# Optimization experiments

Measured on AMD Instinct MI355X. Metric: run time of the kernel, lower is better.

Reference implementation:

```python
import jax, jax.numpy as jnp
import numpy as np

NUM_HEADS = 16


def setup_inputs() -> dict:
    key = jax.random.key(0)
    ks = jax.random.split(key, 4)
    B, C, T, D = 1, 1, 3072, 1024
    s = 1.0 / np.sqrt(D)
    return {
        "x": jax.random.normal(ks[0], (B, C, T, D), dtype=jnp.float32),
        "Wq": jax.random.normal(ks[1], (D, D), dtype=jnp.float32) * s,
        "bq": jnp.zeros((D,), dtype=jnp.float32),
        "Wk": jax.random.normal(ks[2], (D, D), dtype=jnp.float32) * s,
        "bk": jnp.zeros((D,), dtype=jnp.float32),
        "Wv": jax.random.normal(ks[3], (D, D), dtype=jnp.float32) * s,
        "bv": jnp.zeros((D,), dtype=jnp.float32),
        "gamma": jnp.float32(0.5),  # learned scalar; 0.0 at torch init, nonzero here for a meaningful signal
    }


def reference(x, Wq, bq, Wk, bk, Wv, bv, gamma):
    # x: (B, C, T, D); Linear acts on last dim (torch: y = x @ W.T + b)
    B, C, T, D = x.shape
    H = NUM_HEADS
    q = (jnp.einsum("bctd,ed->bcte", x, Wq) + bq).reshape(B, -1, T, H)  # (B, X, T, H), X = C*D/H
    k = (jnp.einsum("bctd,ed->bcte", x, Wk) + bk).reshape(B, -1, T, H)
    v = (jnp.einsum("bctd,ed->bcte", x, Wv) + bv).reshape(B, -1, T, H)
    q = q.transpose(0, 3, 2, 1)  # (B, H, T, X)
    k = k.transpose(0, 3, 1, 2)  # (B, H, X, T)
    energy = q @ k               # (B, H, T, T)  -- note: NO 1/sqrt(d) scaling, as in source
    attn = jax.nn.softmax(energy, axis=-1)
    v = v.transpose(0, 3, 2, 1)  # (B, H, T, X)
    out = attn @ v               # (B, H, T, X)
    out = out.transpose(0, 2, 3, 1).reshape(B, T, -1)  # (B, T, X*H) = (B, T, C*D)
    # residual broadcast: (B, T, C*D) + (B, C, T, D); valid since B == C == 1
    return gamma * out + x
```

## Files before the change

### kernel.cpp

```cpp
#include <hip/hip_runtime.h>


typedef _Float16 v8h __attribute__((ext_vector_type(8)));
typedef _Float16 v4h __attribute__((ext_vector_type(4)));
typedef __fp16   v2pk __attribute__((ext_vector_type(2)));
typedef __fp16   v4pk __attribute__((ext_vector_type(4)));
typedef float    v4f __attribute__((ext_vector_type(4)));

#define TSEQ 3072
#define DM   1024
#define NH   16
#define XD   64
#define LOG2E 1.44269504f

__device__ __forceinline__ void async_load16(const void* g, void* l) {
  __builtin_amdgcn_global_load_lds(
      (const __attribute__((address_space(1))) unsigned int*)g,
      (__attribute__((address_space(3))) unsigned int*)l,
      16, 0, 0);
}

__device__ __forceinline__ float fexp2(float x) {
  float r; asm("v_exp_f32 %0, %1" : "=v"(r) : "v"(x)); return r;
}
__device__ __forceinline__ float flog2(float x) {
  float r; asm("v_log_f32 %0, %1" : "=v"(r) : "v"(x)); return r;
}

extern "C" __global__ __launch_bounds__(256) void cvt_kernel(
    const float* __restrict__ x, const float* __restrict__ wq,
    const float* __restrict__ wk, const float* __restrict__ wv,
    _Float16* __restrict__ xb, _Float16* __restrict__ wb)
{
  const int NX4 = (TSEQ * DM) / 4;
  const int NT  = NX4 * 2;
  for (int i = blockIdx.x * blockDim.x + threadIdx.x; i < NT;
       i += gridDim.x * blockDim.x) {
    float4 v;
    _Float16* dst;
    if (i < NX4) {
      v = ((const float4*)x)[i];
      dst = xb + (size_t)i * 4;
    } else {
      const int j = i - NX4;
      const int n = j >> 8;
      if (n < 1024)      v = ((const float4*)wq)[j];
      else if (n < 2048) v = ((const float4*)wk)[j - 262144];
      else               v = ((const float4*)wv)[j - 524288];
      dst = wb + (size_t)j * 4;
    }
    v4h h;
    h[0] = (_Float16)v.x; h[1] = (_Float16)v.y;
    h[2] = (_Float16)v.z; h[3] = (_Float16)v.w;
    *(v4h*)dst = h;
  }
}

extern "C" __global__ __launch_bounds__(256) void qkv_gemm_kernel(
    const _Float16* __restrict__ xb, const _Float16* __restrict__ wb,
    const float* __restrict__ bq, const float* __restrict__ bk,
    const float* __restrict__ bv,
    _Float16* __restrict__ qlin, _Float16* __restrict__ klin,
    _Float16* __restrict__ vlin)
{
  __shared__ _Float16 As[128 * 32];
  __shared__ _Float16 Bs[128 * 32];
  const int tid = threadIdx.x;
  const int w = tid >> 6, l = tid & 63;
  const int li = l & 15, lg = l >> 4;
  const int wm = w >> 1, wn = w & 1;
  const int bid = blockIdx.x;
  const int swz = (bid & 7) * 72 + (bid >> 3);
  const int m0 = (swz / 24) * 128, n0 = (swz % 24) * 128;
  v4f acc[4][4] = {};
  const int srow = l >> 2;
  const int scol = (l & 3) * 8;
  for (int k0 = 0; k0 < DM; k0 += 32) {
#pragma unroll
    for (int c = 0; c < 2; ++c) {
      const int rbase = c * 64 + w * 16;
      async_load16(xb + (size_t)(m0 + rbase + srow) * DM + k0 + scol, &As[rbase * 32]);
      async_load16(wb + (size_t)(n0 + rbase + srow) * DM + k0 + scol, &Bs[rbase * 32]);
    }
    __syncthreads();
    v8h af[4], bf[4];
#pragma unroll
    for (int mi = 0; mi < 4; ++mi)
      af[mi] = *(const v8h*)&As[(wm * 64 + mi * 16 + li) * 32 + lg * 8];
#pragma unroll
    for (int ni = 0; ni < 4; ++ni)
      bf[ni] = *(const v8h*)&Bs[(wn * 64 + ni * 16 + li) * 32 + lg * 8];
#pragma unroll
    for (int mi = 0; mi < 4; ++mi)
#pragma unroll
      for (int ni = 0; ni < 4; ++ni)
        acc[mi][ni] = __builtin_amdgcn_mfma_f32_16x16x32_f16(
            af[mi], bf[ni], acc[mi][ni], 0, 0, 0);
    __syncthreads();
  }
  const int which = n0 >> 10;
  const int ebase = n0 & 1023;
  const float* bias = which == 0 ? bq : (which == 1 ? bk : bv);
  _Float16* outp = which == 0 ? qlin : (which == 1 ? klin : vlin);
#pragma unroll
  for (int mi = 0; mi < 4; ++mi)
#pragma unroll
    for (int r = 0; r < 4; ++r) {
      const int t = m0 + wm * 64 + mi * 16 + lg * 4 + r;
#pragma unroll
      for (int ni = 0; ni < 4; ++ni) {
        const int e = ebase + wn * 64 + ni * 16 + li;
        outp[(size_t)t * DM + e] = (_Float16)(acc[mi][ni][r] + bias[e]);
      }
    }
}

extern "C" __global__ __launch_bounds__(256) void repack_kernel(
    const _Float16* __restrict__ qlin, const _Float16* __restrict__ klin,
    const _Float16* __restrict__ vlin,
    _Float16* __restrict__ qh, _Float16* __restrict__ kh,
    _Float16* __restrict__ vt)
{
  const int NE = NH * TSEQ * XD;
  for (int g = blockIdx.x * blockDim.x + threadIdx.x; g < 3 * NE;
       g += gridDim.x * blockDim.x) {
    if (g < 2 * NE) {
      const int gg = (g < NE) ? g : g - NE;
      const int xx = gg & 63;
      const int rest = gg >> 6;
      const int h = rest / TSEQ;
      const int i = rest - h * TSEQ;
      const int t = xx * 48 + (i >> 6);
      const int e = ((i & 63) << 4) + h;
      if (g < NE) qh[gg] = qlin[t * DM + e];
      else        kh[gg] = (_Float16)((float)klin[t * DM + e] * LOG2E);
    } else {
      const int o = g - 2 * NE;
      const int j = o % TSEQ;
      const int rest = o / TSEQ;
      const int xx = rest & 63;
      const int h = rest >> 6;
      const int t = xx * 48 + (j >> 6);
      const int e = ((j & 63) << 4) + h;
      vt[o] = vlin[t * DM + e];
    }
  }
}

extern "C" __global__ __launch_bounds__(512, 2) void attn_kernel(
    const _Float16* __restrict__ qh, const _Float16* __restrict__ kh,
    const _Float16* __restrict__ vt,
    _Float16* __restrict__ oP0, _Float16* __restrict__ oP1,
    float* __restrict__ sml0, float* __restrict__ sml1)
{
  __shared__ _Float16 SH[8192];
  const int tid = threadIdx.x;
  const int w = tid >> 6, l = tid & 63;
  const int li = l & 15, lg = l >> 4;
  const int b = blockIdx.x;
  const int r = b >> 3;
  const int head = (b & 7) + 8 * (r & 1);
  const int qt = (r >> 1) & 7;
  const int jh = r >> 4;
  const int i0 = qt * 384;
  const size_t hb = (size_t)head * TSEQ * XD;
  _Float16* oPart = jh ? oP1 : oP0;
  float* smlp = jh ? sml1 : sml0;

  v8h qf[3][2];
#pragma unroll
  for (int ct = 0; ct < 3; ++ct) {
    const _Float16* qrow = qh + hb + (size_t)(i0 + w * 48 + ct * 16 + li) * XD;
    qf[ct][0] = *(const v8h*)(qrow + lg * 8);
    qf[ct][1] = *(const v8h*)(qrow + 32 + lg * 8);
  }
  float m2[3] = {24.0f * LOG2E, 24.0f * LOG2E, 24.0f * LOG2E};
  float l4[3] = {0.0f, 0.0f, 0.0f};
  v4f oacc[4][3] = {};
  const int r8 = l >> 3, c8 = l & 7;
  const int jbase = jh * 1536;

  for (int j0 = jbase; j0 < jbase + 1536; j0 += 64) {
    {
      const int row = w * 8 + r8;
      async_load16(kh + hb + (size_t)(j0 + row) * XD + ((c8 ^ (row & 7)) * 8),
                   &SH[w * 512]);
      async_load16(vt + hb + (size_t)row * TSEQ + j0 + ((c8 ^ (row & 7)) * 8),
                   &SH[4096 + w * 512]);
    }
    __syncthreads();
    const _Float16* Kc = &SH[0];
    const _Float16* Vc = &SH[4096];

    v4f e4[3][4];
#pragma unroll
    for (int kt = 0; kt < 4; ++kt) {
      const int krow = kt * 16 + li;
      const v8h kf0 = *(const v8h*)&Kc[krow * 64 + ((lg ^ (li & 7)) * 8)];
      const v8h kf1 = *(const v8h*)&Kc[krow * 64 + (((4 + lg) ^ (li & 7)) * 8)];
#pragma unroll
      for (int ct = 0; ct < 3; ++ct) {
        v4f a = {-m2[ct], -m2[ct], -m2[ct], -m2[ct]};
        a = __builtin_amdgcn_mfma_f32_16x16x32_f16(kf0, qf[ct][0], a, 0, 0, 0);
        a = __builtin_amdgcn_mfma_f32_16x16x32_f16(kf1, qf[ct][1], a, 0, 0, 0);
        e4[ct][kt] = a;
      }
    }

    float gm = -1.0e30f;
#pragma unroll
    for (int ct = 0; ct < 3; ++ct)
#pragma unroll
      for (int kt = 0; kt < 4; ++kt)
        gm = fmaxf(fmaxf(gm, fmaxf(e4[ct][kt][0], e4[ct][kt][1])),
                   fmaxf(e4[ct][kt][2], e4[ct][kt][3]));
    if (__any(gm > 11.5f)) {
#pragma unroll
      for (int ct = 0; ct < 3; ++ct) {
        float rm = -1.0e30f;
#pragma unroll
        for (int kt = 0; kt < 4; ++kt)
          rm = fmaxf(fmaxf(rm, fmaxf(e4[ct][kt][0], e4[ct][kt][1])),
                     fmaxf(e4[ct][kt][2], e4[ct][kt][3]));
        rm = fmaxf(rm, __shfl_xor(rm, 16, 64));
        rm = fmaxf(rm, __shfl_xor(rm, 32, 64));
        rm = fmaxf(rm, 0.0f);
        const float fs = fexp2(-rm);
#pragma unroll
        for (int kt = 0; kt < 4; ++kt)
#pragma unroll
          for (int rr = 0; rr < 4; ++rr) e4[ct][kt][rr] -= rm;
        l4[ct] *= fs;
#pragma unroll
        for (int mi = 0; mi < 4; ++mi) oacc[mi][ct] *= fs;
        m2[ct] += rm;
      }
    }

    v4h pv[3][4];
#pragma unroll
    for (int ct = 0; ct < 3; ++ct) {
#pragma unroll
      for (int kt = 0; kt < 4; ++kt) {
        const float p0 = fexp2(e4[ct][kt][0]);
        const float p1 = fexp2(e4[ct][kt][1]);
        const float p2 = fexp2(e4[ct][kt][2]);
        const float p3 = fexp2(e4[ct][kt][3]);
        const v2pk lo = __builtin_amdgcn_cvt_pkrtz(p0, p1);
        const v2pk hi = __builtin_amdgcn_cvt_pkrtz(p2, p3);
        const v4pk pk = __builtin_shufflevector(lo, hi, 0, 1, 2, 3);
        pv[ct][kt] = __builtin_bit_cast(v4h, pk);
        l4[ct] += (p0 + p1) + (p2 + p3);
      }
    }

#pragma unroll
    for (int mi = 0; mi < 4; ++mi) {
      const int vrow = mi * 16 + li;
      const int vb = vrow * 64 + (lg & 1) * 4;
#pragma unroll
      for (int kt = 0; kt < 4; ++kt) {
        const v4h vf = *(const v4h*)&Vc[vb + (((kt * 2 + (lg >> 1)) ^ (li & 7)) * 8)];
#pragma unroll
        for (int ct = 0; ct < 3; ++ct)
          oacc[mi][ct] = __builtin_amdgcn_mfma_f32_16x16x16f16(
              vf, pv[ct][kt], oacc[mi][ct], 0, 0, 0);
      }
    }
    __syncthreads();
  }

#pragma unroll
  for (int ct = 0; ct < 3; ++ct) {
    float ls = l4[ct];
    ls += __shfl_xor(ls, 16, 64);
    ls += __shfl_xor(ls, 32, 64);
    const float inv = 1.0f / ls;
    const int rl = w * 48 + ct * 16 + li;
    if (lg == 0) smlp[(size_t)(i0 + rl) * NH + head] = m2[ct] + flog2(ls);
#pragma unroll
    for (int mi = 0; mi < 4; ++mi) {
      v4h o4;
#pragma unroll
      for (int rr = 0; rr < 4; ++rr) o4[rr] = (_Float16)(oacc[mi][ct][rr] * inv);
      *(v4h*)&oPart[(size_t)(i0 + rl) * DM + head * 64 + mi * 16 + lg * 4] = o4;
    }
  }
}

extern "C" __global__ __launch_bounds__(256) void epilogue_kernel(
    const _Float16* __restrict__ oP0, const _Float16* __restrict__ oP1,
    const float* __restrict__ sml0, const float* __restrict__ sml1,
    const float* __restrict__ xin, const float* __restrict__ gscal,
    float* __restrict__ outp)
{
  __shared__ float po[8 * 1024];
  const int tid = threadIdx.x;
  const size_t t0 = (size_t)blockIdx.x * 8;
  {
    const int tr = tid >> 5;
    const int c0 = (tid & 31) * 32;
    const int h = c0 >> 6;
    const size_t t = t0 + tr;
    const float s0 = sml0[t * NH + h], s1 = sml1[t * NH + h];
    const float M = fmaxf(s0, s1);
    float u0 = fexp2(s0 - M), u1 = fexp2(s1 - M);
    const float dn = 1.0f / (u0 + u1);
    u0 *= dn; u1 *= dn;
    const _Float16* p0 = oP0 + t * DM + c0;
    const _Float16* p1 = oP1 + t * DM + c0;
#pragma unroll
    for (int c = 0; c < 4; ++c) {
      const v8h a = *(const v8h*)(p0 + c * 8);
      const v8h bb = *(const v8h*)(p1 + c * 8);
#pragma unroll
      for (int e = 0; e < 8; ++e)
        po[tr * 1024 + c0 + c * 8 + e] = u0 * (float)a[e] + u1 * (float)bb[e];
    }
  }
  __syncthreads();
  const float g = gscal[0];
  const int tr = tid >> 5;
  const int d0 = (tid & 31) * 32;
  const size_t rb = (t0 + tr) * DM + d0;
#pragma unroll
  for (int c4 = 0; c4 < 8; ++c4) {
    const float4 xi = *(const float4*)&xin[rb + c4 * 4];
    float4 rr;
    rr.x = g * po[tr * 1024 + ((c4 * 4 + 0) & 15) * 64 + ((d0 + c4 * 4 + 0) >> 4)] + xi.x;
    rr.y = g * po[tr * 1024 + ((c4 * 4 + 1) & 15) * 64 + ((d0 + c4 * 4 + 1) >> 4)] + xi.y;
    rr.z = g * po[tr * 1024 + ((c4 * 4 + 2) & 15) * 64 + ((d0 + c4 * 4 + 2) >> 4)] + xi.z;
    rr.w = g * po[tr * 1024 + ((c4 * 4 + 3) & 15) * 64 + ((d0 + c4 * 4 + 3) >> 4)] + xi.w;
    *(float4*)&outp[rb + c4 * 4] = rr;
  }
}

extern "C" void kernel_launch(void* const* d_in, const int* in_sizes, int n_in,
                              void* d_out, int out_size, void* d_ws, size_t ws_size,
                              hipStream_t stream)
{
  const float* x  = (const float*)d_in[0];
  const float* Wq = (const float*)d_in[1];
  const float* bq = (const float*)d_in[2];
  const float* Wk = (const float*)d_in[3];
  const float* bk = (const float*)d_in[4];
  const float* Wv = (const float*)d_in[5];
  const float* bv = (const float*)d_in[6];
  const float* gm = (const float*)d_in[7];
  float* outp = (float*)d_out;
  char* ws = (char*)d_ws;
  const size_t SZH = (size_t)TSEQ * DM * sizeof(_Float16);
  _Float16* xb   = (_Float16*)(ws);
  _Float16* wb   = (_Float16*)(ws + SZH);
  _Float16* qlin = (_Float16*)(ws + 2 * SZH);
  _Float16* klin = (_Float16*)(ws + 3 * SZH);
  _Float16* vlin = (_Float16*)(ws + 4 * SZH);
  _Float16* qhp  = (_Float16*)(ws + 5 * SZH);
  _Float16* khp  = (_Float16*)(ws + 6 * SZH);
  _Float16* vtp  = (_Float16*)(ws + 7 * SZH);
  _Float16* oP0  = (_Float16*)(ws);
  _Float16* oP1  = (_Float16*)(ws + SZH);
  float*    sml0 = (float*)(ws + 3 * SZH);
  float*    sml1 = sml0 + (size_t)TSEQ * NH;

  cvt_kernel<<<dim3(1024), dim3(256), 0, stream>>>(x, Wq, Wk, Wv, xb, wb);
  qkv_gemm_kernel<<<dim3(576), dim3(256), 0, stream>>>(xb, wb, bq, bk, bv,
                                                       qlin, klin, vlin);
  repack_kernel<<<dim3(4096), dim3(256), 0, stream>>>(qlin, klin, vlin,
                                                      qhp, khp, vtp);
  attn_kernel<<<dim3(256), dim3(512), 0, stream>>>(qhp, khp, vtp,
                                                   oP0, oP1, sml0, sml1);
  epilogue_kernel<<<dim3(384), dim3(256), 0, stream>>>(oP0, oP1, sml0, sml1,
                                                       x, gm, outp);
  (void)in_sizes; (void)n_in; (void)out_size; (void)ws_size;
}
```

Measured before the change: 137.7 us.

## Fuse head repack into QKV GEMM epilogue and halve attention block size

The QKV GEMM epilogue now writes Q, K (pre-scaled by log2e) and transposed V straight into the per-head attention layouts, so the separate repack kernel and its intermediate buffers are gone. This removes one launch and a full read-write pass over the Q/K/V tensors, at the cost of scattered, uncoalesced stores from the GEMM. The attention kernel also moves from 512-thread blocks over 384 query rows to 256-thread blocks over 192 rows, with twice as many blocks and each thread issuing two async K/V tile loads. The workspace layout is adjusted so the softmax statistics buffers reuse the freed space.

Result: slower. 180.9 us (+31.4%).

```diff
diff --git a/kernel.cpp b/kernel.cpp
--- a/kernel.cpp
+++ b/kernel.cpp
@@ -60,8 +60,8 @@
     const _Float16* __restrict__ xb, const _Float16* __restrict__ wb,
     const float* __restrict__ bq, const float* __restrict__ bk,
     const float* __restrict__ bv,
-    _Float16* __restrict__ qlin, _Float16* __restrict__ klin,
-    _Float16* __restrict__ vlin)
+    _Float16* __restrict__ qh, _Float16* __restrict__ kh,
+    _Float16* __restrict__ vt)
 {
   __shared__ _Float16 As[128 * 32];
   __shared__ _Float16 Bs[128 * 32];
@@ -101,53 +101,31 @@
   const int which = n0 >> 10;
   const int ebase = n0 & 1023;
   const float* bias = which == 0 ? bq : (which == 1 ? bk : bv);
-  _Float16* outp = which == 0 ? qlin : (which == 1 ? klin : vlin);
+  const float scale = (which == 1) ? LOG2E : 1.0f;
+  const int h = li;
 #pragma unroll
   for (int mi = 0; mi < 4; ++mi)
 #pragma unroll
     for (int r = 0; r < 4; ++r) {
       const int t = m0 + wm * 64 + mi * 16 + lg * 4 + r;
+      const int tq = t / 48;
+      const int ib = (t - tq * 48) * 64;
 #pragma unroll
       for (int ni = 0; ni < 4; ++ni) {
         const int e = ebase + wn * 64 + ni * 16 + li;
-        outp[(size_t)t * DM + e] = (_Float16)(acc[mi][ni][r] + bias[e]);
-      }
-    }
-}
-
-extern "C" __global__ __launch_bounds__(256) void repack_kernel(
-    const _Float16* __restrict__ qlin, const _Float16* __restrict__ klin,
-    const _Float16* __restrict__ vlin,
-    _Float16* __restrict__ qh, _Float16* __restrict__ kh,
-    _Float16* __restrict__ vt)
-{
-  const int NE = NH * TSEQ * XD;
-  for (int g = blockIdx.x * blockDim.x + threadIdx.x; g < 3 * NE;
-       g += gridDim.x * blockDim.x) {
-    if (g < 2 * NE) {
-      const int gg = (g < NE) ? g : g - NE;
-      const int xx = gg & 63;
-      const int rest = gg >> 6;
-      const int h = rest / TSEQ;
-      const int i = rest - h * TSEQ;
-      const int t = xx * 48 + (i >> 6);
-      const int e = ((i & 63) << 4) + h;
-      if (g < NE) qh[gg] = qlin[t * DM + e];
-      else        kh[gg] = (_Float16)((float)klin[t * DM + e] * LOG2E);
-    } else {
-      const int o = g - 2 * NE;
-      const int j = o % TSEQ;
-      const int rest = o / TSEQ;
-      const int xx = rest & 63;
-      const int h = rest >> 6;
-      const int t = xx * 48 + (j >> 6);
-      const int e = ((j & 63) << 4) + h;
-      vt[o] = vlin[t * DM + e];
-    }
-  }
-}
-
-extern "C" __global__ __launch_bounds__(512, 2) void attn_kernel(
+        const int colq = (ebase >> 4) + wn * 4 + ni;
+        const float v = (acc[mi][ni][r] + bias[e]) * scale;
+        if (which == 2)
+          vt[((size_t)h * XD + tq) * TSEQ + ib + colq] = (_Float16)v;
+        else if (which == 0)
+          qh[(size_t)h * TSEQ * XD + (size_t)(ib + colq) * XD + tq] = (_Float16)v;
+        else
+          kh[(size_t)h * TSEQ * XD + (size_t)(ib + colq) * XD + tq] = (_Float16)v;
+      }
+    }
+}
+
+extern "C" __global__ __launch_bounds__(256, 2) void attn_kernel(
     const _Float16* __restrict__ qh, const _Float16* __restrict__ kh,
     const _Float16* __restrict__ vt,
     _Float16* __restrict__ oP0, _Float16* __restrict__ oP1,
@@ -158,11 +136,11 @@
   const int w = tid >> 6, l = tid & 63;
   const int li = l & 15, lg = l >> 4;
   const int b = blockIdx.x;
-  const int r = b >> 3;
-  const int head = (b & 7) + 8 * (r & 1);
-  const int qt = (r >> 1) & 7;
-  const int jh = r >> 4;
-  const int i0 = qt * 384;
+  const int rest = b >> 3;
+  const int head = (b & 7) + 8 * (rest & 1);
+  const int qt = (rest >> 1) & 15;
+  const int jh = rest >> 5;
+  const int i0 = qt * 192;
   const size_t hb = (size_t)head * TSEQ * XD;
   _Float16* oPart = jh ? oP1 : oP0;
   float* smlp = jh ? sml1 : sml0;
@@ -181,12 +159,14 @@
   const int jbase = jh * 1536;
 
   for (int j0 = jbase; j0 < jbase + 1536; j0 += 64) {
-    {
-      const int row = w * 8 + r8;
+#pragma unroll
+    for (int s = 0; s < 2; ++s) {
+      const int n = w * 2 + s;
+      const int row = n * 8 + r8;
       async_load16(kh + hb + (size_t)(j0 + row) * XD + ((c8 ^ (row & 7)) * 8),
-                   &SH[w * 512]);
+                   &SH[n * 512]);
       async_load16(vt + hb + (size_t)row * TSEQ + j0 + ((c8 ^ (row & 7)) * 8),
-                   &SH[4096 + w * 512]);
+                   &SH[4096 + n * 512]);
     }
     __syncthreads();
     const _Float16* Kc = &SH[0];
@@ -352,23 +332,18 @@
   const size_t SZH = (size_t)TSEQ * DM * sizeof(_Float16);
   _Float16* xb   = (_Float16*)(ws);
   _Float16* wb   = (_Float16*)(ws + SZH);
-  _Float16* qlin = (_Float16*)(ws + 2 * SZH);
-  _Float16* klin = (_Float16*)(ws + 3 * SZH);
-  _Float16* vlin = (_Float16*)(ws + 4 * SZH);
+  float*    sml0 = (float*)(ws + 2 * SZH);
+  float*    sml1 = sml0 + (size_t)TSEQ * NH;
   _Float16* qhp  = (_Float16*)(ws + 5 * SZH);
   _Float16* khp  = (_Float16*)(ws + 6 * SZH);
   _Float16* vtp  = (_Float16*)(ws + 7 * SZH);
   _Float16* oP0  = (_Float16*)(ws);
   _Float16* oP1  = (_Float16*)(ws + SZH);
-  float*    sml0 = (float*)(ws + 3 * SZH);
-  float*    sml1 = sml0 + (size_t)TSEQ * NH;
 
   cvt_kernel<<<dim3(1024), dim3(256), 0, stream>>>(x, Wq, Wk, Wv, xb, wb);
   qkv_gemm_kernel<<<dim3(576), dim3(256), 0, stream>>>(xb, wb, bq, bk, bv,
-                                                       qlin, klin, vlin);
-  repack_kernel<<<dim3(4096), dim3(256), 0, stream>>>(qlin, klin, vlin,
-                                                      qhp, khp, vtp);
-  attn_kernel<<<dim3(256), dim3(512), 0, stream>>>(qhp, khp, vtp,
+                                                       qhp, khp, vtp);
+  attn_kernel<<<dim3(512), dim3(256), 0, stream>>>(qhp, khp, vtp,
                                                    oP0, oP1, sml0, sml1);
   epilogue_kernel<<<dim3(384), dim3(256), 0, stream>>>(oP0, oP1, sml0, sml1,
                                                        x, gm, outp);
```
